# Kernel optimization log

Measured on AMD Instinct MI355X. Metric: run time of the kernel, lower is better.

Reference implementation:

```python
import jax, jax.numpy as jnp
import numpy as np

EMBED_DIM = 512
N_HEAD = 8
Q_DIM = 64
V_DIM = 64
WINDOW_SIZE = 3


def setup_inputs() -> dict:
    key = jax.random.key(0)
    ks = jax.random.split(key, 9)
    B, N = 2, 2048
    x = jax.random.normal(ks[0], (B, N, EMBED_DIM), dtype=jnp.float32)
    s = 0.02
    # torch nn.Linear weights are [out_features, in_features]; y = x @ W.T + b
    Wq = jax.random.normal(ks[1], (N_HEAD * Q_DIM, EMBED_DIM), dtype=jnp.float32) * s
    bq = jax.random.normal(ks[2], (N_HEAD * Q_DIM,), dtype=jnp.float32) * s
    Wk = jax.random.normal(ks[3], (N_HEAD * Q_DIM, EMBED_DIM), dtype=jnp.float32) * s
    bk = jax.random.normal(ks[4], (N_HEAD * Q_DIM,), dtype=jnp.float32) * s
    Wv = jax.random.normal(ks[5], (N_HEAD * V_DIM, EMBED_DIM), dtype=jnp.float32) * s
    bv = jax.random.normal(ks[6], (N_HEAD * V_DIM,), dtype=jnp.float32) * s
    Wo = jax.random.normal(ks[7], (EMBED_DIM, N_HEAD * V_DIM), dtype=jnp.float32) * s
    bo = jax.random.normal(ks[8], (EMBED_DIM,), dtype=jnp.float32) * s
    return {"x": x, "Wq": Wq, "bq": bq, "Wk": Wk, "bk": bk,
            "Wv": Wv, "bv": bv, "Wo": Wo, "bo": bo}


def _diag_indices(n_seq, di):
    # rows i and cols j = i + di of the di-th diagonal
    if di >= 0:
        ii = np.arange(0, n_seq - di)
    else:
        ii = np.arange(-di, n_seq)
    return ii, ii + di


def reference(x, Wq, bq, Wk, bk, Wv, bv, Wo, bo):
    B, N, E = x.shape
    H, Dq, Dv = N_HEAD, Q_DIM, V_DIM
    Q = (x @ Wq.T + bq).reshape(B, N, H, Dq).transpose(0, 2, 1, 3)  # [B,H,N,Dq]
    K = (x @ Wk.T + bk).reshape(B, N, H, Dq).transpose(0, 2, 1, 3)
    V = (x @ Wv.T + bv).reshape(B, N, H, Dv).transpose(0, 2, 1, 3)  # [B,H,N,Dv]
    half = WINDOW_SIZE // 2
    # Faithful to source: scores scattered into COLUMN index i (the loop
    # counter), not the key position; all other columns remain 0 and still
    # participate in the full softmax over n_seq.
    columns = jnp.zeros((B, H, N, N), dtype=x.dtype)
    for i, di in enumerate(range(-half, half + 1)):
        ii, jj = _diag_indices(N, di)
        c = jnp.einsum('bhid,bhid->bhi', Q[:, :, ii, :], K[:, :, jj, :])
        columns = columns.at[:, :, ii, i].set(c)
    attn = jax.nn.softmax(columns, axis=-1)          # [B,H,N,N]
    out = attn @ V                                    # [B,H,N,Dv]
    out = out.transpose(0, 2, 1, 3).reshape(B, N, H * Dv)
    return out @ Wo.T + bo
```

## Files before the change

### kernel.cpp

```cpp
#include <hip/hip_runtime.h>
#include <hip/hip_bf16.h>

#define EMBED 512
#define NSEQ 2048
#define NROWS 4096

typedef unsigned short u16;
typedef __bf16 bf16x8 __attribute__((ext_vector_type(8)));
typedef float f32x4 __attribute__((ext_vector_type(4)));
typedef unsigned short ushort8 __attribute__((ext_vector_type(8)));

__device__ __forceinline__ u16 f2bf(float f) {
    unsigned u = __float_as_uint(f);
    unsigned r = (u + 0x7FFFu + ((u >> 16) & 1u)) >> 16;
    return (u16)r;
}
__device__ __forceinline__ float bf2f(u16 v) {
    return __uint_as_float((unsigned)v << 16);
}

#define XELEMS    (NROWS * EMBED)
#define WQKELEMS  (1024 * EMBED)

__global__ __launch_bounds__(256) void prep_kernel(
    const float* __restrict__ x,
    const float* __restrict__ Wq, const float* __restrict__ Wk,
    u16* __restrict__ xb, u16* __restrict__ Wcat,
    float* __restrict__ xcs_part)
{
    __shared__ float cs[4][512];
    const int bid = blockIdx.x, t = threadIdx.x;
    if (bid < 256) {
        const float* src = x + (size_t)bid * 16 * EMBED;
        u16* dst = xb + (size_t)bid * 16 * EMBED;
        const int rl = t >> 6;
        const int co = (t & 63) * 8;
        float s0=0.f,s1=0.f,s2=0.f,s3=0.f,s4=0.f,s5=0.f,s6=0.f,s7=0.f;
#pragma unroll
        for (int i = 0; i < 4; ++i) {
            const size_t off = (size_t)(i * 4 + rl) * EMBED + co;
            float4 a = *(const float4*)(src + off);
            float4 b = *(const float4*)(src + off + 4);
            union { u16 u[8]; uint4 v; } p;
            p.u[0]=f2bf(a.x); p.u[1]=f2bf(a.y); p.u[2]=f2bf(a.z); p.u[3]=f2bf(a.w);
            p.u[4]=f2bf(b.x); p.u[5]=f2bf(b.y); p.u[6]=f2bf(b.z); p.u[7]=f2bf(b.w);
            *(uint4*)(dst + off) = p.v;
            s0+=a.x; s1+=a.y; s2+=a.z; s3+=a.w;
            s4+=b.x; s5+=b.y; s6+=b.z; s7+=b.w;
        }
        f32x4 v0 = {s0,s1,s2,s3}, v1 = {s4,s5,s6,s7};
        *(f32x4*)&cs[rl][co]     = v0;
        *(f32x4*)&cs[rl][co + 4] = v1;
        __syncthreads();
        const int b = bid >> 7, blk = bid & 127;
#pragma unroll
        for (int d = t; d < 512; d += 256) {
            xcs_part[((size_t)b * 128 + blk) * 512 + d] =
                cs[0][d] + cs[1][d] + cs[2][d] + cs[3][d];
        }
    } else {
        const long long e0 = (long long)(bid - 256) * 2048 + (long long)t * 8;
        const int row = (int)(e0 >> 9), col = (int)(e0 & 511);
        const float* src = (row < 512) ? (Wq + (size_t)row * EMBED + col)
                                       : (Wk + (size_t)(row - 512) * EMBED + col);
        float4 a = *(const float4*)(src);
        float4 b = *(const float4*)(src + 4);
        union { u16 u[8]; uint4 v; } p;
        p.u[0]=f2bf(a.x); p.u[1]=f2bf(a.y); p.u[2]=f2bf(a.z); p.u[3]=f2bf(a.w);
        p.u[4]=f2bf(b.x); p.u[5]=f2bf(b.y); p.u[6]=f2bf(b.z); p.u[7]=f2bf(b.w);
        *(uint4*)(Wcat + e0) = p.v;
    }
}

__global__ __launch_bounds__(256) void gemm_qk_mfma(
    const u16* __restrict__ A, const u16* __restrict__ W,
    const float* __restrict__ bq, const float* __restrict__ bk,
    const float* __restrict__ xcs_part, const float* __restrict__ bv,
    const float* __restrict__ Wv, const float* __restrict__ Wo,
    u16* __restrict__ QKb, float* __restrict__ WT)
{
    __shared__ __align__(16) u16 As[2 * 128 * 64];
    __shared__ __align__(16) u16 Bs[2 * 64 * 64];
    const int t = threadIdx.x;

    if (blockIdx.x < 32) {
        float* xcs  = (float*)As;
        float* Vraw = (float*)Bs;
        float* Vloc = Vraw + 256;
        const int sid = blockIdx.x;
        const int b = sid >> 4, h = (sid >> 1) & 7, jhalf = sid & 1;

        {
            const float* p = xcs_part + (size_t)b * 128 * 512 + 2 * t;
            float a0 = 0.f, a1 = 0.f, c0 = 0.f, c1 = 0.f;
#pragma unroll 4
            for (int blk = 0; blk < 128; blk += 2) {
                float2 u = *(const float2*)(p + (size_t)blk * 512);
                float2 v = *(const float2*)(p + (size_t)(blk + 1) * 512);
                a0 += u.x; a1 += u.y; c0 += v.x; c1 += v.y;
            }
            xcs[2 * t] = a0 + c0; xcs[2 * t + 1] = a1 + c1;
        }
        __syncthreads();

        const int tt = t >> 6, cl = t & 63;
        const int col = h * 64 + cl;
        const float* wv = Wv + (size_t)col * EMBED;
        float r = 0.f;
        if (tt < 3) {
            const u16* xr = A + ((size_t)b * NSEQ + tt) * EMBED;
#pragma unroll 8
            for (int d = 0; d < EMBED; d += 8) {
                ushort8 xv = *(const ushort8*)(xr + d);
                f32x4 w0 = *(const f32x4*)(wv + d);
                f32x4 w1 = *(const f32x4*)(wv + d + 4);
                r = fmaf(bf2f(xv[0]), w0[0], r);
                r = fmaf(bf2f(xv[1]), w0[1], r);
                r = fmaf(bf2f(xv[2]), w0[2], r);
                r = fmaf(bf2f(xv[3]), w0[3], r);
                r = fmaf(bf2f(xv[4]), w1[0], r);
                r = fmaf(bf2f(xv[5]), w1[1], r);
                r = fmaf(bf2f(xv[6]), w1[2], r);
                r = fmaf(bf2f(xv[7]), w1[3], r);
            }
        } else {
#pragma unroll 8
            for (int d = 0; d < EMBED; d += 4) {
                f32x4 w = *(const f32x4*)(wv + d);
                r = fmaf(xcs[d],     w[0], r);
                r = fmaf(xcs[d + 1], w[1], r);
                r = fmaf(xcs[d + 2], w[2], r);
                r = fmaf(xcs[d + 3], w[3], r);
            }
        }
        Vraw[tt * 64 + cl] = r;
        __syncthreads();
        const float bvc = bv[col];
        if (tt < 3) Vloc[tt * 64 + cl] = r + bvc;
        else        Vloc[192 + cl] = r - (Vraw[cl] + Vraw[64 + cl] + Vraw[128 + cl])
                                       + 2045.f * bvc;
        __syncthreads();

        const int j = jhalf * 256 + t;
        const float* wo = Wo + (size_t)j * EMBED + h * 64;
        float a0 = 0.f, a1 = 0.f, a2 = 0.f, a3 = 0.f;
#pragma unroll
        for (int c = 0; c < 64; c += 4) {
            f32x4 w = *(const f32x4*)(wo + c);
#pragma unroll
            for (int z = 0; z < 4; ++z) {
                a0 = fmaf(Vloc[c + z],       w[z], a0);
                a1 = fmaf(Vloc[64 + c + z],  w[z], a1);
                a2 = fmaf(Vloc[128 + c + z], w[z], a2);
                a3 = fmaf(Vloc[192 + c + z], w[z], a3);
            }
        }
        float* wt = WT + ((size_t)b * 512 + j) * 32 + h * 4;
        wt[0] = a0; wt[1] = a1; wt[2] = a2; wt[3] = a3;
        return;
    }

    const int bb = blockIdx.x - 32;
    const int m0 = (bb & 31) * 128;
    const int n0 = (bb >> 5) * 64;
    const int sel = n0 >> 9;
    const float* bias = ((sel == 0) ? bq : bk) + (n0 & 511);

    const int wave = t >> 6, lane = t & 63;
    const int wm   = wave >> 1, wn = wave & 1;
    const int qd   = lane >> 4, lr = lane & 15;

    const int sr8 = lane >> 3;
    const int sg  = (lane & 7) ^ sr8;
    const int soff = sg * 8;

    f32x4 acc[4][2] = {};

    const u16* Asrc = A + (size_t)m0 * EMBED + (size_t)(wave * 8 + sr8) * EMBED + soff;
    const u16* Bsrc = W + (size_t)n0 * EMBED + (size_t)(wave * 8 + sr8) * EMBED + soff;

    u16* Ad0 = As + (size_t)(wave * 8) * 64;
    u16* Bd0 = Bs + (size_t)(wave * 8) * 64;

#define STAGE(bufi, kc)                                                          \
    do {                                                                         \
        u16* Ad = Ad0 + (bufi) * (128 * 64);                                     \
        u16* Bd = Bd0 + (bufi) * (64 * 64);                                      \
        _Pragma("unroll")                                                        \
        for (int j = 0; j < 4; ++j)                                              \
            __builtin_amdgcn_global_load_lds(                                    \
                (const __attribute__((address_space(1))) void*)(Asrc + (kc) + (size_t)j * 32 * EMBED), \
                (__attribute__((address_space(3))) void*)(Ad + j * 32 * 64), 16, 0, 0); \
        _Pragma("unroll")                                                        \
        for (int j = 0; j < 2; ++j)                                              \
            __builtin_amdgcn_global_load_lds(                                    \
                (const __attribute__((address_space(1))) void*)(Bsrc + (kc) + (size_t)j * 32 * EMBED), \
                (__attribute__((address_space(3))) void*)(Bd + j * 32 * 64), 16, 0, 0); \
    } while (0)

    STAGE(0, 0);
    __syncthreads();

    int cur = 0;
#pragma unroll
    for (int ki = 0; ki < 8; ++ki) {
        if (ki < 7) STAGE(cur ^ 1, (ki + 1) * 64);

        const u16* Ab = As + cur * (128 * 64);
        const u16* Bb = Bs + cur * (64 * 64);
#pragma unroll
        for (int kk = 0; kk < 2; ++kk) {
            const int gr = ((kk * 4 + qd) ^ (lr & 7)) * 8;
            bf16x8 af[4], bfr[2];
#pragma unroll
            for (int i = 0; i < 4; ++i)
                af[i]  = *(const bf16x8*)&Ab[(wm * 64 + i * 16 + lr) * 64 + gr];
#pragma unroll
            for (int i = 0; i < 2; ++i)
                bfr[i] = *(const bf16x8*)&Bb[(wn * 32 + i * 16 + lr) * 64 + gr];
#pragma unroll
            for (int mi = 0; mi < 4; ++mi)
#pragma unroll
                for (int ni = 0; ni < 2; ++ni)
                    acc[mi][ni] = __builtin_amdgcn_mfma_f32_16x16x32_bf16(
                        af[mi], bfr[ni], acc[mi][ni], 0, 0, 0);
        }
        if (ki < 7) __syncthreads();
        cur ^= 1;
    }
#undef STAGE

#pragma unroll
    for (int ni = 0; ni < 2; ++ni) {
        const int cl = wn * 32 + ni * 16 + lr;
        const float bb2 = bias[cl];
#pragma unroll
        for (int mi = 0; mi < 4; ++mi)
#pragma unroll
            for (int e = 0; e < 4; ++e) {
                const int row = m0 + wm * 64 + mi * 16 + qd * 4 + e;
                QKb[(size_t)row * 1024 + n0 + cl] = f2bf(acc[mi][ni][e] + bb2);
            }
    }
}

__global__ __launch_bounds__(256) void attn_out_kernel(
    const u16* __restrict__ QKb, const float* __restrict__ WT,
    const float* __restrict__ bo, float* __restrict__ out)
{
    __shared__ float E[16][32];
    const int r0   = blockIdx.x * 16;
    const int b    = r0 >> 11;
    const int wave = threadIdx.x >> 6, lane = threadIdx.x & 63;
    const int d0   = lane * 8;

#pragma unroll
    for (int i = 0; i < 4; ++i) {
        const int rl = wave * 4 + i;
        const int r  = r0 + rl;
        const int sr = r & (NSEQ - 1);
        const u16* Qr = QKb + (size_t)r * 1024 + d0;
        const u16* Kr = QKb + (size_t)r * 1024 + 512 + d0;

        ushort8 qv = *(const ushort8*)Qr;
        ushort8 kv = *(const ushort8*)Kr;
        float q[8], k[8];
#pragma unroll
        for (int z = 0; z < 8; ++z) { q[z] = bf2f(qv[z]); k[z] = bf2f(kv[z]); }

        float s1 = 0.f;
#pragma unroll
        for (int z = 0; z < 8; ++z) s1 = fmaf(q[z], k[z], s1);

        float s0 = 0.f, s2 = 0.f;
        if (sr > 0) {
            ushort8 pv = *(const ushort8*)(Kr - 1024);
#pragma unroll
            for (int z = 0; z < 8; ++z) s0 = fmaf(q[z], bf2f(pv[z]), s0);
        }
        if (sr < NSEQ - 1) {
            ushort8 nv = *(const ushort8*)(Kr + 1024);
#pragma unroll
            for (int z = 0; z < 8; ++z) s2 = fmaf(q[z], bf2f(nv[z]), s2);
        }
#pragma unroll
        for (int off = 1; off <= 4; off <<= 1) {
            s0 += __shfl_xor(s0, off);
            s1 += __shfl_xor(s1, off);
            s2 += __shfl_xor(s2, off);
        }
        const float m  = fmaxf(fmaxf(s0, s1), fmaxf(s2, 0.f));
        const float e0 = __expf(s0 - m);
        const float e1 = __expf(s1 - m);
        const float e2 = __expf(s2 - m);
        const float eb = __expf(-m);
        const float rd = 1.f / (e0 + e1 + e2 + (float)(NSEQ - 3) * eb);
        const int h = lane >> 3, jj = lane & 7;
        const float coef = (jj == 0) ? e0 : (jj == 1) ? e1 : (jj == 2) ? e2 : eb;
        if (jj < 4) E[rl][h * 4 + jj] = coef * rd;
    }
    __syncthreads();

    const int j0 = threadIdx.x * 2;
    const float* WTb = WT + (size_t)b * 512 * 32;
    float w0[32], w1[32];
#pragma unroll
    for (int s = 0; s < 32; ++s) {
        w0[s] = WTb[(size_t)j0 * 32 + s];
        w1[s] = WTb[(size_t)(j0 + 1) * 32 + s];
    }
    const float b0 = bo[j0], b1 = bo[j0 + 1];
#pragma unroll
    for (int rl = 0; rl < 16; ++rl) {
        float a0 = b0, a1 = b1;
#pragma unroll
        for (int s = 0; s < 32; ++s) {
            const float e = E[rl][s];
            a0 = fmaf(e, w0[s], a0);
            a1 = fmaf(e, w1[s], a1);
        }
        *(float2*)(out + (size_t)(r0 + rl) * EMBED + j0) = make_float2(a0, a1);
    }
}

extern "C" void kernel_launch(void* const* d_in, const int* in_sizes, int n_in,
                              void* d_out, int out_size, void* d_ws, size_t ws_size,
                              hipStream_t stream)
{
    const float* x  = (const float*)d_in[0];
    const float* Wq = (const float*)d_in[1];
    const float* bq = (const float*)d_in[2];
    const float* Wk = (const float*)d_in[3];
    const float* bk = (const float*)d_in[4];
    const float* Wv = (const float*)d_in[5];
    const float* bv = (const float*)d_in[6];
    const float* Wo = (const float*)d_in[7];
    const float* bo = (const float*)d_in[8];
    float* out = (float*)d_out;

    u16*   QKb      = (u16*)d_ws;
    u16*   xb       = QKb + (size_t)NROWS * 1024;
    u16*   Wcat     = xb + XELEMS;
    float* xcs_part = (float*)(Wcat + WQKELEMS);
    float* WT       = xcs_part + 2 * 128 * 512;

    prep_kernel<<<512, 256, 0, stream>>>(x, Wq, Wk, xb, Wcat, xcs_part);
    gemm_qk_mfma<<<544, 256, 0, stream>>>(xb, Wcat, bq, bk, xcs_part, bv, Wv, Wo,
                                          QKb, WT);
    attn_out_kernel<<<256, 256, 0, stream>>>(QKb, WT, bo, out);
}
```

Baseline: 117.6 us.

## Shrink QK GEMM tile to 64x64 and drop LDS double buffering

Changes the QK projection GEMM from 128x64 tiles with double-buffered LDS staging to 64x64 tiles with a single buffer and a sync before and after each K chunk. The grid grows from 544 to 1056 blocks to fill more CUs and raise occupancy through smaller LDS use. The cost is less operand reuse per tile and no overlap between global-to-LDS loads and MFMA compute.

```diff
diff --git a/kernel.cpp b/kernel.cpp
--- a/kernel.cpp
+++ b/kernel.cpp
@@ -79,8 +79,8 @@
     const float* __restrict__ Wv, const float* __restrict__ Wo,
     u16* __restrict__ QKb, float* __restrict__ WT)
 {
-    __shared__ __align__(16) u16 As[2 * 128 * 64];
-    __shared__ __align__(16) u16 Bs[2 * 64 * 64];
+    __shared__ __align__(16) u16 As[64 * 64];
+    __shared__ __align__(16) u16 Bs[64 * 64];
     const int t = threadIdx.x;
 
     if (blockIdx.x < 32) {
@@ -161,8 +161,8 @@
     }
 
     const int bb = blockIdx.x - 32;
-    const int m0 = (bb & 31) * 128;
-    const int n0 = (bb >> 5) * 64;
+    const int m0 = (bb & 63) * 64;
+    const int n0 = (bb >> 6) * 64;
     const int sel = n0 >> 9;
     const float* bias = ((sel == 0) ? bq : bk) + (n0 & 511);
 
@@ -174,71 +174,54 @@
     const int sg  = (lane & 7) ^ sr8;
     const int soff = sg * 8;
 
-    f32x4 acc[4][2] = {};
-
-    const u16* Asrc = A + (size_t)m0 * EMBED + (size_t)(wave * 8 + sr8) * EMBED + soff;
-    const u16* Bsrc = W + (size_t)n0 * EMBED + (size_t)(wave * 8 + sr8) * EMBED + soff;
-
-    u16* Ad0 = As + (size_t)(wave * 8) * 64;
-    u16* Bd0 = Bs + (size_t)(wave * 8) * 64;
-
-#define STAGE(bufi, kc)                                                          \
-    do {                                                                         \
-        u16* Ad = Ad0 + (bufi) * (128 * 64);                                     \
-        u16* Bd = Bd0 + (bufi) * (64 * 64);                                      \
-        _Pragma("unroll")                                                        \
-        for (int j = 0; j < 4; ++j)                                              \
-            __builtin_amdgcn_global_load_lds(                                    \
-                (const __attribute__((address_space(1))) void*)(Asrc + (kc) + (size_t)j * 32 * EMBED), \
-                (__attribute__((address_space(3))) void*)(Ad + j * 32 * 64), 16, 0, 0); \
-        _Pragma("unroll")                                                        \
-        for (int j = 0; j < 2; ++j)                                              \
-            __builtin_amdgcn_global_load_lds(                                    \
-                (const __attribute__((address_space(1))) void*)(Bsrc + (kc) + (size_t)j * 32 * EMBED), \
-                (__attribute__((address_space(3))) void*)(Bd + j * 32 * 64), 16, 0, 0); \
-    } while (0)
-
-    STAGE(0, 0);
-    __syncthreads();
-
-    int cur = 0;
-#pragma unroll
-    for (int ki = 0; ki < 8; ++ki) {
-        if (ki < 7) STAGE(cur ^ 1, (ki + 1) * 64);
-
-        const u16* Ab = As + cur * (128 * 64);
-        const u16* Bb = Bs + cur * (64 * 64);
+    f32x4 acc[2][2] = {};
+
+    const u16* Asrc = A + ((size_t)m0 + wave * 8 + sr8) * EMBED + soff;
+    const u16* Bsrc = W + ((size_t)n0 + wave * 8 + sr8) * EMBED + soff;
+    u16* Adst = As + (size_t)(wave * 8) * 64;
+    u16* Bdst = Bs + (size_t)(wave * 8) * 64;
+
+    for (int kc = 0; kc < EMBED; kc += 64) {
+#pragma unroll
+        for (int j = 0; j < 2; ++j) {
+            __builtin_amdgcn_global_load_lds(
+                (const __attribute__((address_space(1))) void*)(Asrc + kc + (size_t)j * 32 * EMBED),
+                (__attribute__((address_space(3))) void*)(Adst + j * 32 * 64), 16, 0, 0);
+            __builtin_amdgcn_global_load_lds(
+                (const __attribute__((address_space(1))) void*)(Bsrc + kc + (size_t)j * 32 * EMBED),
+                (__attribute__((address_space(3))) void*)(Bdst + j * 32 * 64), 16, 0, 0);
+        }
+        __syncthreads();
+
 #pragma unroll
         for (int kk = 0; kk < 2; ++kk) {
             const int gr = ((kk * 4 + qd) ^ (lr & 7)) * 8;
-            bf16x8 af[4], bfr[2];
-#pragma unroll
-            for (int i = 0; i < 4; ++i)
-                af[i]  = *(const bf16x8*)&Ab[(wm * 64 + i * 16 + lr) * 64 + gr];
+            bf16x8 af[2], bfr[2];
 #pragma unroll
             for (int i = 0; i < 2; ++i)
-                bfr[i] = *(const bf16x8*)&Bb[(wn * 32 + i * 16 + lr) * 64 + gr];
-#pragma unroll
-            for (int mi = 0; mi < 4; ++mi)
+                af[i]  = *(const bf16x8*)&As[(wm * 32 + i * 16 + lr) * 64 + gr];
+#pragma unroll
+            for (int i = 0; i < 2; ++i)
+                bfr[i] = *(const bf16x8*)&Bs[(wn * 32 + i * 16 + lr) * 64 + gr];
+#pragma unroll
+            for (int mi = 0; mi < 2; ++mi)
 #pragma unroll
                 for (int ni = 0; ni < 2; ++ni)
                     acc[mi][ni] = __builtin_amdgcn_mfma_f32_16x16x32_bf16(
                         af[mi], bfr[ni], acc[mi][ni], 0, 0, 0);
         }
-        if (ki < 7) __syncthreads();
-        cur ^= 1;
-    }
-#undef STAGE
+        __syncthreads();
+    }
 
 #pragma unroll
     for (int ni = 0; ni < 2; ++ni) {
         const int cl = wn * 32 + ni * 16 + lr;
         const float bb2 = bias[cl];
 #pragma unroll
-        for (int mi = 0; mi < 4; ++mi)
+        for (int mi = 0; mi < 2; ++mi)
 #pragma unroll
             for (int e = 0; e < 4; ++e) {
-                const int row = m0 + wm * 64 + mi * 16 + qd * 4 + e;
+                const int row = m0 + wm * 32 + mi * 16 + qd * 4 + e;
                 QKb[(size_t)row * 1024 + n0 + cl] = f2bf(acc[mi][ni][e] + bb2);
             }
     }
@@ -345,7 +328,7 @@
     float* WT       = xcs_part + 2 * 128 * 512;
 
     prep_kernel<<<512, 256, 0, stream>>>(x, Wq, Wk, xb, Wcat, xcs_part);
-    gemm_qk_mfma<<<544, 256, 0, stream>>>(xb, Wcat, bq, bk, xcs_part, bv, Wv, Wo,
-                                          QKb, WT);
+    gemm_qk_mfma<<<1056, 256, 0, stream>>>(xb, Wcat, bq, bk, xcs_part, bv, Wv, Wo,
+                                           QKb, WT);
     attn_out_kernel<<<256, 256, 0, stream>>>(QKb, WT, bo, out);
 }
```

New measurement: 116.0 us. Within noise of the previous version (-1.4%).
